# Kernel tuning notes

Hardware: AMD Instinct MI355X
Metric: run time of the kernel (lower is better)

## Reference

```python
import jax, jax.numpy as jnp
import numpy as np
from jax import lax

EPS = 1e-5  # BatchNorm / LayerNorm eps
B, DIM, H, W = 32, 256, 64, 64
S = 64            # state_dim
D_INNER = 256     # ssd_expand * dim
HIDDEN = 1024     # mlp_ratio * dim


def _bn(x, g, b, m, v):
    # BatchNorm2d, inference mode with given running stats. x: (B,C,H,W)
    inv = lax.rsqrt(v + EPS)
    return (x - m[None, :, None, None]) * (g * inv)[None, :, None, None] + b[None, :, None, None]


def _dwconv3x3(x, w):
    # depthwise 3x3 conv, stride 1, SAME padding. w: (C,1,3,3)
    return lax.conv_general_dilated(
        x, w, window_strides=(1, 1), padding='SAME',
        feature_group_count=x.shape[1],
        dimension_numbers=('NCHW', 'OIHW', 'NCHW'))


def setup_inputs() -> dict:
    key = jax.random.key(0)
    ks = jax.random.split(key, 32)
    n = lambda i, shp, s=0.02: jax.random.normal(ks[i], shp, jnp.float32) * s
    u = lambda i, shp: jax.random.uniform(ks[i], shp, jnp.float32)
    return {
        'x': jax.random.normal(ks[0], (B, DIM, H, W), jnp.float32),
        # dwconv1 (Conv2dNorm depthwise)
        'dw1_w': n(1, (DIM, 1, 3, 3)), 'dw1_g': 1.0 + n(2, (DIM,)), 'dw1_b': n(3, (DIM,)),
        'dw1_m': n(4, (DIM,)), 'dw1_v': u(5, (DIM,)) + 0.5,
        # LayerNorm1d
        'ln_w': 1.0 + n(6, (DIM,)), 'ln_b': n(7, (DIM,)),
        # mixer (HSMSSD)
        'bcdt_w': n(8, (3 * S, DIM)),
        'dwm_w': n(9, (3 * S, 1, 3, 3)),
        'A_param': 1.0 + 15.0 * u(10, (S,)),
        'hz_w': n(11, (2 * D_INNER, DIM)),
        'out_w': n(12, (DIM, D_INNER)),
        'D_param': jnp.ones((1,), jnp.float32),
        # dwconv2
        'dw2_w': n(13, (DIM, 1, 3, 3)), 'dw2_g': 1.0 + n(14, (DIM,)), 'dw2_b': n(15, (DIM,)),
        'dw2_m': n(16, (DIM,)), 'dw2_v': u(17, (DIM,)) + 0.5,
        # FFN
        'fc1_w': n(18, (HIDDEN, DIM)), 'fc1_g': 1.0 + n(19, (HIDDEN,)), 'fc1_b': n(20, (HIDDEN,)),
        'fc1_m': n(21, (HIDDEN,)), 'fc1_v': u(22, (HIDDEN,)) + 0.5,
        'fc2_w': n(23, (DIM, HIDDEN)), 'fc2_g': 1.0 + n(24, (DIM,)), 'fc2_b': n(25, (DIM,)),
        'fc2_m': n(26, (DIM,)), 'fc2_v': u(27, (DIM,)) + 0.5,
        # alpha-gated residual blends
        'alpha': 1e-4 * jnp.ones((4, DIM), jnp.float32) + n(28, (4, DIM), 0.01),
    }


def reference(x, dw1_w, dw1_g, dw1_b, dw1_m, dw1_v, ln_w, ln_b,
              bcdt_w, dwm_w, A_param, hz_w, out_w, D_param,
              dw2_w, dw2_g, dw2_b, dw2_m, dw2_v,
              fc1_w, fc1_g, fc1_b, fc1_m, fc1_v,
              fc2_w, fc2_g, fc2_b, fc2_m, fc2_v, alpha):
    b, dim, h_, w_ = x.shape
    L = h_ * w_
    a = jax.nn.sigmoid(alpha)[:, :, None, None]  # (4, dim, 1, 1)

    # alpha-blended depthwise conv 1
    x = (1.0 - a[0]) * x + a[0] * _bn(_dwconv3x3(x, dw1_w), dw1_g, dw1_b, dw1_m, dw1_v)
    x_prev = x

    # LayerNorm1d over channel dim on (B, C, L)
    xf = x.reshape(b, dim, L)
    mean = xf.mean(axis=1, keepdims=True)
    var = ((xf - mean) ** 2).mean(axis=1, keepdims=True)
    xn = (xf - mean) * lax.rsqrt(var + EPS) * ln_w[None, :, None] + ln_b[None, :, None]

    # HSMSSD mixer
    bc_dt = jnp.einsum('bcl,oc->bol', xn, bcdt_w).reshape(b, 3 * S, h_, w_)
    bc_dt = _dwconv3x3(bc_dt, dwm_w).reshape(b, 3 * S, L)
    Bm, Cm, dt = jnp.split(bc_dt, 3, axis=1)          # each (B, S, L)
    Am = jax.nn.softmax(dt + A_param[None, :, None], axis=-1)
    AB = Am * Bm                                      # (B, S, L)
    h = jnp.einsum('bcl,bsl->bcs', xn, AB)            # (B, dim, S)
    hz = jnp.einsum('bcs,oc->bos', h, hz_w)           # (B, 2*d_inner, S)
    hh, z = jnp.split(hz, 2, axis=1)
    hg = hh * jax.nn.silu(z) + hh * D_param[0]
    hout = jnp.einsum('bcs,oc->bos', hg, out_w)       # (B, dim, S)
    y = jnp.einsum('bcs,bsl->bcl', hout, Cm).reshape(b, dim, h_, w_)

    x = (1.0 - a[1]) * x_prev + a[1] * y
    x = (1.0 - a[2]) * x + a[2] * _bn(_dwconv3x3(x, dw2_w), dw2_g, dw2_b, dw2_m, dw2_v)

    # FFN: 1x1 conv + BN + ReLU + 1x1 conv + BN
    t = _bn(jnp.einsum('bchw,oc->bohw', x, fc1_w), fc1_g, fc1_b, fc1_m, fc1_v)
    t = jax.nn.relu(t)
    t = _bn(jnp.einsum('bchw,oc->bohw', t, fc2_w), fc2_g, fc2_b, fc2_m, fc2_v)
    x = (1.0 - a[3]) * x + a[3] * t
    return (x, hout)
```

## Files before the change

kernel.cpp:

```cpp
#include <hip/hip_runtime.h>
#include <hip/hip_bf16.h>

typedef __hip_bfloat16 bf16;
typedef __attribute__((ext_vector_type(8))) short bf16x8;
typedef __attribute__((ext_vector_type(4))) float f32x4;

__device__ __forceinline__ float LD(const float* p){ return *p; }
__device__ __forceinline__ float LD(const bf16* p){ return __bfloat162float(*p); }
__device__ __forceinline__ void ST(float* p, float v){ *p = v; }
__device__ __forceinline__ void ST(bf16* p, float v){ *p = __float2bfloat16(v); }
__device__ __forceinline__ float sigm(float v){ return 1.f/(1.f + expf(-v)); }
__device__ __forceinline__ ushort f2b(float f){
    unsigned u = __float_as_uint(f);
    return (ushort)((u + 0x7fffu + ((u>>16)&1u)) >> 16);
}

#define NEPS 1e-5f

__global__ __launch_bounds__(256) void dwconv_bn_blend(
        const float* __restrict__ xin, float* __restrict__ xout,
        const float* __restrict__ w, const float* __restrict__ gg, const float* __restrict__ bb,
        const float* __restrict__ mm, const float* __restrict__ vv,
        const float* __restrict__ alpha, int arow)
{
    __shared__ float tile[66*66];
    int blk = blockIdx.x;
    int ch = blk & 255;
    const float* xp = xin + (size_t)blk*4096;
    float* op = xout + (size_t)blk*4096;
    int tid = threadIdx.x;
    for (int i = tid; i < 66*66; i += 256) {
        int r = i/66, c = i%66;
        int gr = r-1, gc = c-1;
        float val = 0.f;
        if (gr >= 0 && gr < 64 && gc >= 0 && gc < 64) val = xp[gr*64+gc];
        tile[i] = val;
    }
    __syncthreads();
    float wv[9];
    #pragma unroll
    for (int k=0;k<9;k++) wv[k] = w[ch*9+k];
    float sc = gg[ch] * rsqrtf(vv[ch] + NEPS);
    float mv = mm[ch], bv = bb[ch];
    float av = sigm(alpha[arow*256+ch]);
    for (int p = tid; p < 4096; p += 256) {
        int r = p>>6, c = p&63;
        float a = 0.f;
        #pragma unroll
        for (int dr=0;dr<3;dr++)
            #pragma unroll
            for (int dc=0;dc<3;dc++)
                a += wv[dr*3+dc]*tile[(r+dr)*66 + (c+dc)];
        float bn = (a - mv)*sc + bv;
        float xv = tile[(r+1)*66 + (c+1)];
        op[p] = (1.f-av)*xv + av*bn;
    }
}

__global__ __launch_bounds__(256) void ln_stats(const float* __restrict__ x1,
        float* __restrict__ meanp, float* __restrict__ invp)
{
    int blk = blockIdx.x;
    int b = blk >> 4;
    int l = ((blk & 15) << 8) + threadIdx.x;
    const float* xp = x1 + (size_t)b*256*4096 + l;
    float mean = 0.f, m2 = 0.f;
    for (int c=0;c<256;c++){ float v = xp[(size_t)c*4096]; mean += v; m2 += v*v; }
    mean *= (1.f/256.f); m2 *= (1.f/256.f);
    meanp[b*4096 + l] = mean;
    invp[b*4096 + l] = rsqrtf(m2 - mean*mean + NEPS);
}

__global__ __launch_bounds__(256) void prep_k(
        const float* __restrict__ f1w, const float* __restrict__ f2w,
        const float* __restrict__ bcdtw,
        const float* __restrict__ g1, const float* __restrict__ b1,
        const float* __restrict__ m1, const float* __restrict__ v1,
        const float* __restrict__ g2, const float* __restrict__ b2,
        const float* __restrict__ m2, const float* __restrict__ v2,
        ushort* __restrict__ w1bf, ushort* __restrict__ w2bf,
        ushort* __restrict__ wbc,
        float* __restrict__ sc1, float* __restrict__ sb1,
        float* __restrict__ sc2, float* __restrict__ sb2)
{
    int i = blockIdx.x*256 + threadIdx.x;
    if (i < 262144) {
        w1bf[i] = f2b(f1w[i]);
        w2bf[i] = f2b(f2w[i]);
    }
    if (i < 49152) wbc[i] = f2b(bcdtw[i]);
    if (i < 1024) { float s = g1[i]*rsqrtf(v1[i]+NEPS); sc1[i]=s; sb1[i]=b1[i]-m1[i]*s; }
    if (i < 256)  { float s = g2[i]*rsqrtf(v2[i]+NEPS); sc2[i]=s; sb2[i]=b2[i]-m2[i]*s; }
}

__global__ __launch_bounds__(256) void bcdt_mfma(
        const float* __restrict__ x1,
        const float* __restrict__ meanp, const float* __restrict__ invp,
        const float* __restrict__ lnw, const float* __restrict__ lnb,
        const ushort* __restrict__ wbc,
        bf16* __restrict__ bc, ushort* __restrict__ xn_bf, int b0)
{
    __shared__ __align__(16) ushort Xs[64*256];
    int blk = blockIdx.x;
    int lb = blk >> 6;
    int b  = b0 + lb;
    int l0 = (blk & 63) << 6;
    int tid = threadIdx.x, lane = tid & 63, w = tid >> 6;
    const float* xp = x1 + (size_t)b*256*4096 + l0;
    float mval = meanp[b*4096 + l0 + lane];
    float ival = invp [b*4096 + l0 + lane];
    ushort* xnp = xn_bf + (size_t)lb*256*4096 + l0;

    for (int cc = w*8; cc < 256; cc += 32) {
        ushort u[8];
        #pragma unroll
        for (int j=0;j<8;j++){
            float v = xp[(size_t)(cc+j)*4096 + lane];
            float xn = (v - mval)*ival*lnw[cc+j] + lnb[cc+j];
            u[j] = f2b(xn);
            xnp[(size_t)(cc+j)*4096 + lane] = u[j];
        }
        uint4 pk;
        pk.x = (uint)u[0] | ((uint)u[1]<<16);
        pk.y = (uint)u[2] | ((uint)u[3]<<16);
        pk.z = (uint)u[4] | ((uint)u[5]<<16);
        pk.w = (uint)u[6] | ((uint)u[7]<<16);
        int g = (cc>>3) ^ (lane&7);
        *(uint4*)&Xs[lane*256 + g*8] = pk;
    }
    __syncthreads();

    f32x4 zero4 = {0.f,0.f,0.f,0.f};
    f32x4 acc[3][4];
    #pragma unroll
    for (int m=0;m<3;m++)
        #pragma unroll
        for (int f=0;f<4;f++) acc[m][f] = zero4;

    int hbase = w*48;
    for (int ks=0; ks<8; ks++){
        bf16x8 afr[3];
        #pragma unroll
        for (int m=0;m<3;m++)
            afr[m] = *(const bf16x8*)&wbc[(size_t)(hbase + m*16 + (lane&15))*256
                                          + ks*32 + (lane>>4)*8];
        #pragma unroll
        for (int f=0;f<4;f++){
            int px = f*16 + (lane&15);
            int g = (ks*4 + (lane>>4)) ^ (px&7);
            bf16x8 bfr = *(const bf16x8*)&Xs[px*256 + g*8];
            #pragma unroll
            for (int m=0;m<3;m++)
                acc[m][f] = __builtin_amdgcn_mfma_f32_16x16x32_bf16(afr[m], bfr, acc[m][f], 0,0,0);
        }
    }
    bf16* op = bc + (size_t)lb*192*4096 + l0;
    #pragma unroll
    for (int m=0;m<3;m++)
        #pragma unroll
        for (int r=0;r<4;r++){
            int o = hbase + m*16 + (lane>>4)*4 + r;
            #pragma unroll
            for (int f=0;f<4;f++){
                int px = f*16 + (lane&15);
                op[(size_t)o*4096 + px] = __float2bfloat16(acc[m][f][r]);
            }
        }
}

__global__ __launch_bounds__(256) void dwconv_plain(bf16* __restrict__ data, const float* __restrict__ w)
{
    __shared__ float tile[66*66];
    int blk = blockIdx.x;
    int ch = blk % 192;
    bf16* xp = data + (size_t)blk*4096;
    int tid = threadIdx.x;
    for (int i = tid; i < 66*66; i += 256) {
        int r = i/66, c = i%66;
        int gr = r-1, gc = c-1;
        float val = 0.f;
        if (gr >= 0 && gr < 64 && gc >= 0 && gc < 64) val = LD(&xp[gr*64+gc]);
        tile[i] = val;
    }
    __syncthreads();
    float wv[9];
    #pragma unroll
    for (int k=0;k<9;k++) wv[k] = w[ch*9+k];
    for (int p = tid; p < 4096; p += 256) {
        int r = p>>6, c = p&63;
        float a = 0.f;
        #pragma unroll
        for (int dr=0;dr<3;dr++)
            #pragma unroll
            for (int dc=0;dc<3;dc++)
                a += wv[dr*3+dc]*tile[(r+dr)*66 + (c+dc)];
        ST(&xp[p], a);
    }
}

__global__ __launch_bounds__(256) void softmax_ab(bf16* __restrict__ bc, const float* __restrict__ A)
{
    __shared__ float red[8];
    int blk = blockIdx.x;
    int lb = blk >> 6;
    int s = blk & 63;
    bf16* dtp = bc + ((size_t)lb*192 + 128 + s)*4096;
    bf16* bmp = bc + ((size_t)lb*192 + s)*4096;
    int tid = threadIdx.x;
    float Av = A[s];
    float vals[16];
    float mx = -1e30f;
    #pragma unroll
    for (int i=0;i<16;i++){ vals[i] = LD(&dtp[i*256+tid]) + Av; mx = fmaxf(mx, vals[i]); }
    #pragma unroll
    for (int o=32;o>0;o>>=1) mx = fmaxf(mx, __shfl_down(mx, o));
    int lane = tid & 63, wid = tid >> 6;
    if (lane == 0) red[wid] = mx;
    __syncthreads();
    if (tid == 0) red[4] = fmaxf(fmaxf(red[0],red[1]), fmaxf(red[2],red[3]));
    __syncthreads();
    mx = red[4];
    float sum = 0.f;
    #pragma unroll
    for (int i=0;i<16;i++){ vals[i] = expf(vals[i]-mx); sum += vals[i]; }
    #pragma unroll
    for (int o=32;o>0;o>>=1) sum += __shfl_down(sum, o);
    if (lane == 0) red[wid] = sum;
    __syncthreads();
    if (tid == 0) red[5] = red[0]+red[1]+red[2]+red[3];
    __syncthreads();
    float inv = 1.f/red[5];
    #pragma unroll
    for (int i=0;i<16;i++){
        float ab = vals[i]*inv*LD(&bmp[i*256+tid]);
        ST(&bmp[i*256+tid], ab);
    }
}

__global__ __launch_bounds__(256) void h_mfma(
        const ushort* __restrict__ xn_bf, const bf16* __restrict__ bc,
        float* __restrict__ h_part)
{
    int blk = blockIdx.x;
    int lb = blk >> 3;
    int kz = blk & 7;
    int kbase = kz*512;
    int tid = threadIdx.x, lane = tid & 63, w = tid >> 6;
    const ushort* ap = xn_bf + (size_t)lb*256*4096;
    const ushort* bp = (const ushort*)bc + (size_t)lb*192*4096;
    f32x4 zero4 = {0.f,0.f,0.f,0.f};
    f32x4 acc[4][4];
    #pragma unroll
    for (int m=0;m<4;m++)
        #pragma unroll
        for (int n=0;n<4;n++) acc[m][n] = zero4;

    for (int ks=0; ks<16; ks++){
        int koff = kbase + ks*32 + (lane>>4)*8;
        bf16x8 afr[4], bfr[4];
        #pragma unroll
        for (int m=0;m<4;m++)
            afr[m] = *(const bf16x8*)&ap[(size_t)(w*64 + m*16 + (lane&15))*4096 + koff];
        #pragma unroll
        for (int n=0;n<4;n++)
            bfr[n] = *(const bf16x8*)&bp[(size_t)(n*16 + (lane&15))*4096 + koff];
        #pragma unroll
        for (int m=0;m<4;m++)
            #pragma unroll
            for (int n=0;n<4;n++)
                acc[m][n] = __builtin_amdgcn_mfma_f32_16x16x32_bf16(afr[m], bfr[n], acc[m][n], 0,0,0);
    }
    float* hp = h_part + ((size_t)lb*8 + kz)*16384;
    #pragma unroll
    for (int m=0;m<4;m++)
        #pragma unroll
        for (int n=0;n<4;n++)
            #pragma unroll
            for (int r=0;r<4;r++){
                int c = w*64 + m*16 + (lane>>4)*4 + r;
                int s = n*16 + (lane&15);
                hp[c*64 + s] = acc[m][n][r];
            }
}

__global__ __launch_bounds__(256) void hz_gemm(const float* __restrict__ h_part,
        const float* __restrict__ w, float* __restrict__ hz)
{
    __shared__ float ht[256][64];
    int blk = blockIdx.x; int lb = blk>>3; int o0 = (blk&7)*64;
    int tid = threadIdx.x;
    const float* hp = h_part + (size_t)lb*8*16384;
    for (int i=tid;i<16384;i+=256){
        float s = 0.f;
        #pragma unroll
        for (int k=0;k<8;k++) s += hp[k*16384 + i];
        ht[i>>6][i&63] = s;
    }
    __syncthreads();
    int lane=tid&63, g=tid>>6;
    for (int i4=0;i4<4;i4++){
        int ol = g*16 + i4*4;
        const float* r0 = w + (size_t)(o0+ol)*256;
        const float *r1=r0+256, *r2=r0+512, *r3=r0+768;
        float d0=0.f,d1=0.f,d2=0.f,d3=0.f;
        #pragma unroll 8
        for (int c4=0;c4<64;c4++){
            float x0=ht[c4*4][lane],x1v=ht[c4*4+1][lane],x2v=ht[c4*4+2][lane],x3v=ht[c4*4+3][lane];
            float4 a0=((const float4*)r0)[c4],a1=((const float4*)r1)[c4];
            float4 a2=((const float4*)r2)[c4],a3=((const float4*)r3)[c4];
            d0 += a0.x*x0+a0.y*x1v+a0.z*x2v+a0.w*x3v;
            d1 += a1.x*x0+a1.y*x1v+a1.z*x2v+a1.w*x3v;
            d2 += a2.x*x0+a2.y*x1v+a2.z*x2v+a2.w*x3v;
            d3 += a3.x*x0+a3.y*x1v+a3.z*x2v+a3.w*x3v;
        }
        size_t base = ((size_t)lb*512 + o0 + ol)*64 + lane;
        hz[base]=d0; hz[base+64]=d1; hz[base+128]=d2; hz[base+192]=d3;
    }
}

__global__ void gate_k(const float* __restrict__ hz, float* __restrict__ hg, const float* __restrict__ Dp)
{
    int i = blockIdx.x*256 + threadIdx.x;
    int lb = i >> 14;
    int r = i & 16383;
    const float* hp = hz + (size_t)lb*32768;
    float hh = hp[r], z = hp[16384 + r];
    float sil = z / (1.f + expf(-z));
    hg[i] = hh * (sil + Dp[0]);
}

__global__ __launch_bounds__(256) void out_gemm(const float* __restrict__ hg, const float* __restrict__ w,
        ushort* __restrict__ hout_bf, float* __restrict__ hout_out, int b0)
{
    __shared__ float ht[256][64];
    int blk = blockIdx.x; int lb = blk>>2; int b = b0 + lb; int o0 = (blk&3)*64;
    int tid = threadIdx.x;
    const float* hp = hg + (size_t)lb*16384;
    for (int i=tid;i<16384;i+=256) ht[i>>6][i&63]=hp[i];
    __syncthreads();
    int lane=tid&63, g=tid>>6;
    for (int i4=0;i4<4;i4++){
        int ol = g*16 + i4*4;
        const float* r0 = w + (size_t)(o0+ol)*256;
        const float *r1=r0+256, *r2=r0+512, *r3=r0+768;
        float d0=0.f,d1=0.f,d2=0.f,d3=0.f;
        #pragma unroll 8
        for (int c4=0;c4<64;c4++){
            float x0=ht[c4*4][lane],x1v=ht[c4*4+1][lane],x2v=ht[c4*4+2][lane],x3v=ht[c4*4+3][lane];
            float4 a0=((const float4*)r0)[c4],a1=((const float4*)r1)[c4];
            float4 a2=((const float4*)r2)[c4],a3=((const float4*)r3)[c4];
            d0 += a0.x*x0+a0.y*x1v+a0.z*x2v+a0.w*x3v;
            d1 += a1.x*x0+a1.y*x1v+a1.z*x2v+a1.w*x3v;
            d2 += a2.x*x0+a2.y*x1v+a2.z*x2v+a2.w*x3v;
            d3 += a3.x*x0+a3.y*x1v+a3.z*x2v+a3.w*x3v;
        }
        size_t lbase = ((size_t)lb*256 + o0 + ol)*64 + lane;
        hout_bf[lbase]=f2b(d0); hout_bf[lbase+64]=f2b(d1);
        hout_bf[lbase+128]=f2b(d2); hout_bf[lbase+192]=f2b(d3);
        size_t gbase = ((size_t)b*256 + o0 + ol)*64 + lane;
        hout_out[gbase]=d0; hout_out[gbase+64]=d1;
        hout_out[gbase+128]=d2; hout_out[gbase+192]=d3;
    }
}

__global__ __launch_bounds__(256) void y_mfma(
        const ushort* __restrict__ hout_bf, const bf16* __restrict__ bc,
        float* __restrict__ x1, const float* __restrict__ alpha, int b0)
{
    __shared__ __align__(16) ushort Cs[64*64];
    int blk = blockIdx.x; int lb = blk>>6; int b = b0 + lb; int l0 = (blk&63)<<6;
    int tid = threadIdx.x, lane = tid&63, w = tid>>6;
    const ushort* cp = (const ushort*)bc + ((size_t)lb*192 + 64)*4096 + l0;
    for (int sc = w*8; sc < 64; sc += 32){
        ushort u[8];
        #pragma unroll
        for (int j=0;j<8;j++) u[j] = cp[(size_t)(sc+j)*4096 + lane];
        uint4 pk;
        pk.x = (uint)u[0] | ((uint)u[1]<<16);
        pk.y = (uint)u[2] | ((uint)u[3]<<16);
        pk.z = (uint)u[4] | ((uint)u[5]<<16);
        pk.w = (uint)u[6] | ((uint)u[7]<<16);
        int g = (sc>>3) ^ (lane&7);
        *(uint4*)&Cs[lane*64 + g*8] = pk;
    }
    __syncthreads();

    f32x4 zero4 = {0.f,0.f,0.f,0.f};
    f32x4 acc[4][4];
    #pragma unroll
    for (int m=0;m<4;m++)
        #pragma unroll
        for (int f=0;f<4;f++) acc[m][f] = zero4;

    const ushort* ap = hout_bf + (size_t)lb*256*64;
    #pragma unroll
    for (int ks=0; ks<2; ks++){
        bf16x8 afr[4];
        #pragma unroll
        for (int m=0;m<4;m++)
            afr[m] = *(const bf16x8*)&ap[(size_t)(w*64 + m*16 + (lane&15))*64
                                          + ks*32 + (lane>>4)*8];
        #pragma unroll
        for (int f=0;f<4;f++){
            int px = f*16 + (lane&15);
            int s8 = ks*32 + (lane>>4)*8;
            int g = (s8>>3) ^ (px&7);
            bf16x8 bfr = *(const bf16x8*)&Cs[px*64 + g*8];
            #pragma unroll
            for (int m=0;m<4;m++)
                acc[m][f] = __builtin_amdgcn_mfma_f32_16x16x32_bf16(afr[m], bfr, acc[m][f], 0,0,0);
        }
    }

    float* xpo = x1 + (size_t)b*256*4096 + l0;
    #pragma unroll
    for (int m=0;m<4;m++)
        #pragma unroll
        for (int r=0;r<4;r++){
            int c = w*64 + m*16 + (lane>>4)*4 + r;
            float av = sigm(alpha[256+c]);
            #pragma unroll
            for (int f=0;f<4;f++){
                int px = f*16 + (lane&15);
                float xv = xpo[(size_t)c*4096 + px];
                xpo[(size_t)c*4096 + px] = (1.f-av)*xv + av*acc[m][f][r];
            }
        }
}

__global__ __launch_bounds__(256) void ffn_mfma(
        const float* __restrict__ x,
        const ushort* __restrict__ w1bf,
        const ushort* __restrict__ w2bf,
        const float* __restrict__ sc1, const float* __restrict__ sb1,
        const float* __restrict__ sc2, const float* __restrict__ sb2,
        const float* __restrict__ alpha,
        float* __restrict__ out)
{
    __shared__ __align__(16) ushort Xs[64*256];
    __shared__ __align__(16) ushort Ts[2][64*128];
    int blk = blockIdx.x;
    int b = blk >> 6, l0 = (blk & 63) << 6;
    int tid = threadIdx.x, lane = tid & 63, w = tid >> 6;
    const float* xp = x + (size_t)b*256*4096 + l0;

    for (int cc = w*8; cc < 256; cc += 32) {
        float v[8];
        #pragma unroll
        for (int j=0;j<8;j++) v[j] = xp[(size_t)(cc+j)*4096 + lane];
        uint4 pk;
        pk.x = (uint)f2b(v[0]) | ((uint)f2b(v[1])<<16);
        pk.y = (uint)f2b(v[2]) | ((uint)f2b(v[3])<<16);
        pk.z = (uint)f2b(v[4]) | ((uint)f2b(v[5])<<16);
        pk.w = (uint)f2b(v[6]) | ((uint)f2b(v[7])<<16);
        int g = (cc>>3) ^ (lane&7);
        *(uint4*)&Xs[lane*256 + g*8] = pk;
    }
    __syncthreads();

    f32x4 zero4 = {0.f,0.f,0.f,0.f};
    f32x4 acc2[4][4];
    #pragma unroll
    for (int m=0;m<4;m++)
        #pragma unroll
        for (int f=0;f<4;f++) acc2[m][f] = zero4;
    f32x4 c1[2][4];

    auto gemm1 = [&](int hc){
        #pragma unroll
        for (int m=0;m<2;m++)
            #pragma unroll
            for (int f=0;f<4;f++) c1[m][f] = zero4;
        int hbase = hc + w*32;
        for (int ks = 0; ks < 8; ks++) {
            bf16x8 afr[2];
            #pragma unroll
            for (int m=0;m<2;m++)
                afr[m] = *(const bf16x8*)&w1bf[(size_t)(hbase + m*16 + (lane&15))*256
                                               + ks*32 + (lane>>4)*8];
            #pragma unroll
            for (int f=0;f<4;f++){
                int px = f*16 + (lane&15);
                int g = (ks*4 + (lane>>4)) ^ (px&7);
                bf16x8 bfr = *(const bf16x8*)&Xs[px*256 + g*8];
                #pragma unroll
                for (int m=0;m<2;m++)
                    c1[m][f] = __builtin_amdgcn_mfma_f32_16x16x32_bf16(afr[m], bfr, c1[m][f], 0,0,0);
            }
        }
    };

    auto writeTs = [&](int pp, int hc){
        #pragma unroll
        for (int m=0;m<2;m++){
            int hl0 = w*32 + m*16 + ((lane>>4)<<2);
            int h0 = hc + hl0;
            float s0=sc1[h0], s1=sc1[h0+1], s2=sc1[h0+2], s3=sc1[h0+3];
            float q0=sb1[h0], q1=sb1[h0+1], q2=sb1[h0+2], q3=sb1[h0+3];
            int gbase = hl0>>3;
            #pragma unroll
            for (int f=0;f<4;f++){
                int px = f*16 + (lane&15);
                float t0 = fmaxf(c1[m][f][0]*s0 + q0, 0.f);
                float t1 = fmaxf(c1[m][f][1]*s1 + q1, 0.f);
                float t2 = fmaxf(c1[m][f][2]*s2 + q2, 0.f);
                float t3 = fmaxf(c1[m][f][3]*s3 + q3, 0.f);
                uint2 pk;
                pk.x = (uint)f2b(t0) | ((uint)f2b(t1)<<16);
                pk.y = (uint)f2b(t2) | ((uint)f2b(t3)<<16);
                int g = gbase ^ (px&7);
                *(uint2*)&Ts[pp][px*128 + g*8 + (hl0&7)] = pk;
            }
        }
    };

    auto gemm2 = [&](int pp, int hc){
        int c0 = w*64;
        for (int ks = 0; ks < 4; ks++) {
            bf16x8 afr[4];
            #pragma unroll
            for (int m=0;m<4;m++)
                afr[m] = *(const bf16x8*)&w2bf[(size_t)(c0 + m*16 + (lane&15))*1024
                                               + hc + ks*32 + (lane>>4)*8];
            #pragma unroll
            for (int f=0;f<4;f++){
                int px = f*16 + (lane&15);
                int hl = ks*32 + (lane>>4)*8;
                int g = (hl>>3) ^ (px&7);
                bf16x8 bfr = *(const bf16x8*)&Ts[pp][px*128 + g*8];
                #pragma unroll
                for (int m=0;m<4;m++)
                    acc2[m][f] = __builtin_amdgcn_mfma_f32_16x16x32_bf16(afr[m], bfr, acc2[m][f], 0,0,0);
            }
        }
    };

    gemm1(0);
    writeTs(0, 0);
    __syncthreads();
    int p = 0;
    for (int hc = 128; hc < 1024; hc += 128) {
        gemm1(hc);
        gemm2(p, hc-128);
        writeTs(p^1, hc);
        __syncthreads();
        p ^= 1;
    }
    gemm2(p, 896);

    float* op = out + (size_t)b*256*4096 + l0;
    int c0 = w*64;
    #pragma unroll
    for (int m=0;m<4;m++){
        #pragma unroll
        for (int r=0;r<4;r++){
            int c = c0 + m*16 + (lane>>4)*4 + r;
            float a = sigm(alpha[768+c]);
            float s2 = sc2[c], bb2 = sb2[c];
            #pragma unroll
            for (int f=0;f<4;f++){
                int px = f*16 + (lane&15);
                float t2 = acc2[m][f][r]*s2 + bb2;
                float xv = xp[(size_t)c*4096 + px];
                op[(size_t)c*4096 + px] = (1.f-a)*xv + a*t2;
            }
        }
    }
}

extern "C" void kernel_launch(void* const* d_in, const int* in_sizes, int n_in,
                              void* d_out, int out_size, void* d_ws, size_t ws_size,
                              hipStream_t stream)
{
    (void)in_sizes; (void)n_in; (void)out_size;
    const float* x     = (const float*)d_in[0];
    const float* dw1w  = (const float*)d_in[1];
    const float* dw1g  = (const float*)d_in[2];
    const float* dw1b  = (const float*)d_in[3];
    const float* dw1m  = (const float*)d_in[4];
    const float* dw1v  = (const float*)d_in[5];
    const float* lnw   = (const float*)d_in[6];
    const float* lnb   = (const float*)d_in[7];
    const float* bcdtw = (const float*)d_in[8];
    const float* dwmw  = (const float*)d_in[9];
    const float* Ap    = (const float*)d_in[10];
    const float* hzw   = (const float*)d_in[11];
    const float* outw  = (const float*)d_in[12];
    const float* Dp    = (const float*)d_in[13];
    const float* dw2w  = (const float*)d_in[14];
    const float* dw2g  = (const float*)d_in[15];
    const float* dw2b  = (const float*)d_in[16];
    const float* dw2m  = (const float*)d_in[17];
    const float* dw2v  = (const float*)d_in[18];
    const float* f1w   = (const float*)d_in[19];
    const float* f1g   = (const float*)d_in[20];
    const float* f1b   = (const float*)d_in[21];
    const float* f1m   = (const float*)d_in[22];
    const float* f1v   = (const float*)d_in[23];
    const float* f2w   = (const float*)d_in[24];
    const float* f2g   = (const float*)d_in[25];
    const float* f2b_  = (const float*)d_in[26];
    const float* f2m   = (const float*)d_in[27];
    const float* f2v   = (const float*)d_in[28];
    const float* alpha = (const float*)d_in[29];

    const size_t nx = (size_t)32*256*4096;
    float* x1 = (float*)d_out;
    float* hout_out = x1 + nx;

    char* ws = (char*)d_ws;
    float* meanp = (float*)ws;
    float* invp  = meanp + 131072;
    size_t off = 1048576;
    ushort* w1bf = (ushort*)(ws + off); off += 524288;
    ushort* w2bf = (ushort*)(ws + off); off += 524288;
    ushort* wbc  = (ushort*)(ws + off); off += 98304;
    float* sc1 = (float*)(ws + off); off += 4096;
    float* sb1 = (float*)(ws + off); off += 4096;
    float* sc2 = (float*)(ws + off); off += 1024;
    float* sb2 = (float*)(ws + off); off += 1024;
    off = (off + 255) & ~(size_t)255;
    char* cbase = ws + off;
    size_t avail = ws_size > off ? ws_size - off : 0;

    const size_t perb = 1572864 + 2097152 + 524288 + 131072 + 65536 + 32768;
    int NB = 1;
    for (int nb = 32; nb >= 1; nb >>= 1) if (avail >= (size_t)nb*perb) { NB = nb; break; }

    prep_k<<<1024,256,0,stream>>>(f1w, f2w, bcdtw, f1g,f1b,f1m,f1v, f2g,f2b_,f2m,f2v,
                                  w1bf, w2bf, wbc, sc1, sb1, sc2, sb2);
    dwconv_bn_blend<<<8192,256,0,stream>>>(x, x1, dw1w,dw1g,dw1b,dw1m,dw1v, alpha, 0);
    ln_stats<<<512,256,0,stream>>>(x1, meanp, invp);

    bf16*   bc      = (bf16*)cbase;
    ushort* xn_bf   = (ushort*)(cbase + (size_t)NB*1572864);
    float*  h_part  = (float*)(cbase + (size_t)NB*(1572864 + 2097152));
    float*  hz      = (float*)((char*)h_part + (size_t)NB*524288);
    float*  hg      = (float*)((char*)hz + (size_t)NB*131072);
    ushort* hout_bf = (ushort*)((char*)hg + (size_t)NB*65536);

    for (int b0 = 0; b0 < 32; b0 += NB) {
        bcdt_mfma<<<NB*64,256,0,stream>>>(x1, meanp, invp, lnw, lnb, wbc, bc, xn_bf, b0);
        dwconv_plain<<<NB*192,256,0,stream>>>(bc, dwmw);
        softmax_ab<<<NB*64,256,0,stream>>>(bc, Ap);
        h_mfma<<<NB*8,256,0,stream>>>(xn_bf, bc, h_part);
        hz_gemm<<<NB*8,256,0,stream>>>(h_part, hzw, hz);
        gate_k<<<NB*64,256,0,stream>>>(hz, hg, Dp);
        out_gemm<<<NB*4,256,0,stream>>>(hg, outw, hout_bf, hout_out, b0);
        y_mfma<<<NB*64,256,0,stream>>>(hout_bf, bc, x1, alpha, b0);
    }

    dwconv_bn_blend<<<8192,256,0,stream>>>(x1, x1, dw2w,dw2g,dw2b,dw2m,dw2v, alpha, 2);
    ffn_mfma<<<2048,256,0,stream>>>(x1, w1bf, w2bf, sc1, sb1, sc2, sb2, alpha, x1);
}
```

Before: 803.6 us.

## Pre-transpose FFN input to bf16 pixel-major buffer and drop LDS staging

Adds a transpose kernel that converts x1 to a bf16 pixel-major layout in workspace, so the FFN kernel reads its GEMM1 B-fragments directly from global memory instead of staging them in a 32KB LDS tile. This lowers LDS use (possibly raising occupancy) and removes the strided staging loop at block start. In exchange it adds an extra pass over x1 (read fp32, write bf16) and relies on L2 for repeated fragment reads across the eight hidden chunks. It also fully unrolls the K loop in the bcdt kernel and keeps a fallback FFN kernel (single-buffered) for when workspace is too small.

Result: slower. 895.9 us (+11.5%).

```diff
diff --git a/kernel.cpp b/kernel.cpp
--- a/kernel.cpp
+++ b/kernel.cpp
@@ -138,6 +138,7 @@
         for (int f=0;f<4;f++) acc[m][f] = zero4;
 
     int hbase = w*48;
+    #pragma unroll
     for (int ks=0; ks<8; ks++){
         bf16x8 afr[3];
         #pragma unroll
@@ -428,7 +429,35 @@
         }
 }
 
-__global__ __launch_bounds__(256) void ffn_mfma(
+__global__ __launch_bounds__(256) void transpose_k(const float* __restrict__ x1,
+        ushort* __restrict__ xT)
+{
+    __shared__ ushort T[64*258];
+    int blk = blockIdx.x;
+    int b = blk >> 6, l0 = (blk & 63) << 6;
+    int tid = threadIdx.x;
+    const float* xp = x1 + (size_t)b*256*4096 + l0;
+    for (int i = tid; i < 16384; i += 256){
+        int c = i >> 6, l = i & 63;
+        T[l*258 + c] = f2b(xp[(size_t)c*4096 + l]);
+    }
+    __syncthreads();
+    int l = tid & 63, cseg = (tid >> 6) << 6;
+    ushort* op = xT + ((size_t)b*4096 + l0 + l)*256 + cseg;
+    const ushort* tp = &T[l*258 + cseg];
+    #pragma unroll
+    for (int j=0;j<8;j++){
+        uint4 v;
+        v.x = (uint)tp[j*8+0] | ((uint)tp[j*8+1]<<16);
+        v.y = (uint)tp[j*8+2] | ((uint)tp[j*8+3]<<16);
+        v.z = (uint)tp[j*8+4] | ((uint)tp[j*8+5]<<16);
+        v.w = (uint)tp[j*8+6] | ((uint)tp[j*8+7]<<16);
+        *(uint4*)&op[j*8] = v;
+    }
+}
+
+__global__ __launch_bounds__(256) void ffn_mfma_t(
+        const ushort* __restrict__ xT,
         const float* __restrict__ x,
         const ushort* __restrict__ w1bf,
         const ushort* __restrict__ w2bf,
@@ -437,26 +466,12 @@
         const float* __restrict__ alpha,
         float* __restrict__ out)
 {
-    __shared__ __align__(16) ushort Xs[64*256];
     __shared__ __align__(16) ushort Ts[2][64*128];
     int blk = blockIdx.x;
     int b = blk >> 6, l0 = (blk & 63) << 6;
     int tid = threadIdx.x, lane = tid & 63, w = tid >> 6;
+    const ushort* xtp = xT + ((size_t)b*4096 + l0)*256;
     const float* xp = x + (size_t)b*256*4096 + l0;
-
-    for (int cc = w*8; cc < 256; cc += 32) {
-        float v[8];
-        #pragma unroll
-        for (int j=0;j<8;j++) v[j] = xp[(size_t)(cc+j)*4096 + lane];
-        uint4 pk;
-        pk.x = (uint)f2b(v[0]) | ((uint)f2b(v[1])<<16);
-        pk.y = (uint)f2b(v[2]) | ((uint)f2b(v[3])<<16);
-        pk.z = (uint)f2b(v[4]) | ((uint)f2b(v[5])<<16);
-        pk.w = (uint)f2b(v[6]) | ((uint)f2b(v[7])<<16);
-        int g = (cc>>3) ^ (lane&7);
-        *(uint4*)&Xs[lane*256 + g*8] = pk;
-    }
-    __syncthreads();
 
     f32x4 zero4 = {0.f,0.f,0.f,0.f};
     f32x4 acc2[4][4];
@@ -480,9 +495,8 @@
                                                + ks*32 + (lane>>4)*8];
             #pragma unroll
             for (int f=0;f<4;f++){
-                int px = f*16 + (lane&15);
-                int g = (ks*4 + (lane>>4)) ^ (px&7);
-                bf16x8 bfr = *(const bf16x8*)&Xs[px*256 + g*8];
+                bf16x8 bfr = *(const bf16x8*)&xtp[(size_t)(f*16 + (lane&15))*256
+                                                  + ks*32 + (lane>>4)*8];
                 #pragma unroll
                 for (int m=0;m<2;m++)
                     c1[m][f] = __builtin_amdgcn_mfma_f32_16x16x32_bf16(afr[m], bfr, c1[m][f], 0,0,0);
@@ -547,6 +561,127 @@
         p ^= 1;
     }
     gemm2(p, 896);
+
+    float* op = out + (size_t)b*256*4096 + l0;
+    int c0 = w*64;
+    #pragma unroll
+    for (int m=0;m<4;m++){
+        #pragma unroll
+        for (int r=0;r<4;r++){
+            int c = c0 + m*16 + (lane>>4)*4 + r;
+            float a = sigm(alpha[768+c]);
+            float s2 = sc2[c], bb2 = sb2[c];
+            #pragma unroll
+            for (int f=0;f<4;f++){
+                int px = f*16 + (lane&15);
+                float t2 = acc2[m][f][r]*s2 + bb2;
+                float xv = xp[(size_t)c*4096 + px];
+                op[(size_t)c*4096 + px] = (1.f-a)*xv + a*t2;
+            }
+        }
+    }
+}
+
+__global__ __launch_bounds__(256) void ffn_mfma(
+        const float* __restrict__ x,
+        const ushort* __restrict__ w1bf, const ushort* __restrict__ w2bf,
+        const float* __restrict__ sc1, const float* __restrict__ sb1,
+        const float* __restrict__ sc2, const float* __restrict__ sb2,
+        const float* __restrict__ alpha, float* __restrict__ out)
+{
+    __shared__ __align__(16) ushort Xs[64*256];
+    __shared__ __align__(16) ushort Ts[64*128];
+    int blk = blockIdx.x;
+    int b = blk >> 6, l0 = (blk & 63) << 6;
+    int tid = threadIdx.x, lane = tid & 63, w = tid >> 6;
+    const float* xp = x + (size_t)b*256*4096 + l0;
+
+    for (int cc = w*8; cc < 256; cc += 32) {
+        float v[8];
+        #pragma unroll
+        for (int j=0;j<8;j++) v[j] = xp[(size_t)(cc+j)*4096 + lane];
+        uint4 pk;
+        pk.x = (uint)f2b(v[0]) | ((uint)f2b(v[1])<<16);
+        pk.y = (uint)f2b(v[2]) | ((uint)f2b(v[3])<<16);
+        pk.z = (uint)f2b(v[4]) | ((uint)f2b(v[5])<<16);
+        pk.w = (uint)f2b(v[6]) | ((uint)f2b(v[7])<<16);
+        int g = (cc>>3) ^ (lane&7);
+        *(uint4*)&Xs[lane*256 + g*8] = pk;
+    }
+    __syncthreads();
+
+    f32x4 zero4 = {0.f,0.f,0.f,0.f};
+    f32x4 acc2[4][4];
+    #pragma unroll
+    for (int m=0;m<4;m++)
+        #pragma unroll
+        for (int f=0;f<4;f++) acc2[m][f] = zero4;
+
+    for (int hc = 0; hc < 1024; hc += 128) {
+        int hbase = hc + w*32;
+        f32x4 c1[2][4];
+        #pragma unroll
+        for (int m=0;m<2;m++)
+            #pragma unroll
+            for (int f=0;f<4;f++) c1[m][f] = zero4;
+        for (int ks = 0; ks < 8; ks++) {
+            bf16x8 afr[2];
+            #pragma unroll
+            for (int m=0;m<2;m++)
+                afr[m] = *(const bf16x8*)&w1bf[(size_t)(hbase + m*16 + (lane&15))*256
+                                               + ks*32 + (lane>>4)*8];
+            #pragma unroll
+            for (int f=0;f<4;f++){
+                int px = f*16 + (lane&15);
+                int g = (ks*4 + (lane>>4)) ^ (px&7);
+                bf16x8 bfr = *(const bf16x8*)&Xs[px*256 + g*8];
+                #pragma unroll
+                for (int m=0;m<2;m++)
+                    c1[m][f] = __builtin_amdgcn_mfma_f32_16x16x32_bf16(afr[m], bfr, c1[m][f], 0,0,0);
+            }
+        }
+        __syncthreads();
+        #pragma unroll
+        for (int m=0;m<2;m++){
+            int hl0 = w*32 + m*16 + ((lane>>4)<<2);
+            int h0 = hc + hl0;
+            float s0=sc1[h0], s1=sc1[h0+1], s2=sc1[h0+2], s3=sc1[h0+3];
+            float q0=sb1[h0], q1=sb1[h0+1], q2=sb1[h0+2], q3=sb1[h0+3];
+            int gbase = hl0>>3;
+            #pragma unroll
+            for (int f=0;f<4;f++){
+                int px = f*16 + (lane&15);
+                float t0 = fmaxf(c1[m][f][0]*s0 + q0, 0.f);
+                float t1 = fmaxf(c1[m][f][1]*s1 + q1, 0.f);
+                float t2 = fmaxf(c1[m][f][2]*s2 + q2, 0.f);
+                float t3 = fmaxf(c1[m][f][3]*s3 + q3, 0.f);
+                uint2 pk;
+                pk.x = (uint)f2b(t0) | ((uint)f2b(t1)<<16);
+                pk.y = (uint)f2b(t2) | ((uint)f2b(t3)<<16);
+                int g = gbase ^ (px&7);
+                *(uint2*)&Ts[px*128 + g*8 + (hl0&7)] = pk;
+            }
+        }
+        __syncthreads();
+        int c0 = w*64;
+        for (int ks = 0; ks < 4; ks++) {
+            bf16x8 afr[4];
+            #pragma unroll
+            for (int m=0;m<4;m++)
+                afr[m] = *(const bf16x8*)&w2bf[(size_t)(c0 + m*16 + (lane&15))*1024
+                                               + hc + ks*32 + (lane>>4)*8];
+            #pragma unroll
+            for (int f=0;f<4;f++){
+                int px = f*16 + (lane&15);
+                int hl = ks*32 + (lane>>4)*8;
+                int g = (hl>>3) ^ (px&7);
+                bf16x8 bfr = *(const bf16x8*)&Ts[px*128 + g*8];
+                #pragma unroll
+                for (int m=0;m<4;m++)
+                    acc2[m][f] = __builtin_amdgcn_mfma_f32_16x16x32_bf16(afr[m], bfr, acc2[m][f], 0,0,0);
+            }
+        }
+    }
 
     float* op = out + (size_t)b*256*4096 + l0;
     int c0 = w*64;
@@ -620,10 +755,15 @@
     float* sc2 = (float*)(ws + off); off += 1024;
     float* sb2 = (float*)(ws + off); off += 1024;
     off = (off + 255) & ~(size_t)255;
+
+    const size_t xt_bytes = nx*2;
+    ushort* xT = nullptr;
+    size_t rem = ws_size > off ? ws_size - off : 0;
+    const size_t perb = 1572864 + 2097152 + 524288 + 131072 + 65536 + 32768;
+    if (rem >= xt_bytes + perb) { xT = (ushort*)(ws + off); off += xt_bytes; }
     char* cbase = ws + off;
     size_t avail = ws_size > off ? ws_size - off : 0;
 
-    const size_t perb = 1572864 + 2097152 + 524288 + 131072 + 65536 + 32768;
     int NB = 1;
     for (int nb = 32; nb >= 1; nb >>= 1) if (avail >= (size_t)nb*perb) { NB = nb; break; }
 
@@ -651,5 +791,10 @@
     }
 
     dwconv_bn_blend<<<8192,256,0,stream>>>(x1, x1, dw2w,dw2g,dw2b,dw2m,dw2v, alpha, 2);
-    ffn_mfma<<<2048,256,0,stream>>>(x1, w1bf, w2bf, sc1, sb1, sc2, sb2, alpha, x1);
-}
+    if (xT) {
+        transpose_k<<<2048,256,0,stream>>>(x1, xT);
+        ffn_mfma_t<<<2048,256,0,stream>>>(xT, x1, w1bf, w2bf, sc1, sb1, sc2, sb2, alpha, x1);
+    } else {
+        ffn_mfma<<<2048,256,0,stream>>>(x1, w1bf, w2bf, sc1, sb1, sc2, sb2, alpha, x1);
+    }
+}
```
